# Kernel tuning notes

Measured on AMD Instinct MI355X. Metric: run time of the kernel, lower is better.

## Reference

```python
import jax, jax.numpy as jnp
import numpy as np

B, N, C = 32, 2248, 1024
D = 128            # bottleneck (down_size)
P = 200            # num_prompt_tokens
SCALE = D ** (-0.5)


def setup_inputs() -> dict:
    key = jax.random.key(0)
    k = jax.random.split(key, 5)
    return {
        "x": jax.random.normal(k[0], (B, N, C), dtype=jnp.float32),
        "W_down": jax.random.normal(k[1], (C, D), dtype=jnp.float32) * (C ** -0.5),
        "b_down": jax.random.normal(k[2], (D,), dtype=jnp.float32) * 0.01,
        "W_up": jax.random.normal(k[3], (D, C), dtype=jnp.float32) * (D ** -0.5),
        "b_up": jax.random.normal(k[4], (C,), dtype=jnp.float32) * 0.01,
        "gate": jnp.ones((), dtype=jnp.float32),
    }


def reference(x, W_down, b_down, W_up, b_up, gate):
    # down-projection + exact GELU (torch nn.GELU default is erf-based)
    down = jax.nn.gelu(jnp.einsum('bnc,cd->bnd', x, W_down) + b_down,
                       approximate=False)                      # [B, N, D]
    prompt_down = down[:, :P, :]                               # [B, P, D]
    token_down = down[:, P:, :]                                # [B, N-P, D]
    # prompt-token cross attention
    attn = jax.nn.softmax(
        jnp.einsum('bpd,btd->bpt', prompt_down, token_down) * SCALE, axis=-1)
    prompt_out = jnp.einsum('bpt,btd->bpd', attn, token_down)  # [B, P, D]
    combined = jnp.concatenate([prompt_out, token_down], axis=1)  # [B, N, D]
    up = jnp.einsum('bnd,dc->bnc', combined, W_up) + b_up      # [B, N, C]
    return gate * up
```

## Files before the change

### kernel.cpp

```cpp
#include <hip/hip_runtime.h>
#include <hip/hip_bf16.h>
#include <math.h>

#define B_   32
#define N_   2248
#define C_   1024
#define D_   128
#define P_   200
#define T_   2048
#define M_   (B_ * N_)
#define SCALE_ 0.08838834764831845f

typedef __bf16 bf16;
typedef __bf16 bf16x8 __attribute__((ext_vector_type(8)));
typedef __bf16 bf16x4 __attribute__((ext_vector_type(4)));
typedef float  f32x4  __attribute__((ext_vector_type(4)));
typedef unsigned int u32x4 __attribute__((ext_vector_type(4)));

#define VT_COL(dd, t) ((((((t) >> 3) ^ (((dd) >> 3) & 7)) << 3)) | ((t) & 7))

__device__ __forceinline__ void gl_lds16(const void* g, void* l) {
    __builtin_amdgcn_global_load_lds(
        (const __attribute__((address_space(1))) unsigned int*)g,
        (__attribute__((address_space(3))) unsigned int*)l,
        16, 0, 0);
}

__global__ void k_prep(const float* __restrict__ Wd, const float* __restrict__ Wu,
                       bf16* __restrict__ WtD, bf16* __restrict__ WtU) {
    int i = blockIdx.x * 256 + threadIdx.x;
    if (i >= 131072) return;
    int d = i >> 10, k = i & 1023;
    WtD[i] = (bf16)Wd[k * 128 + d];
    int c = i >> 7, e = i & 127;
    WtU[i] = (bf16)Wu[e * 1024 + c];
}

__launch_bounds__(256, 3)
__global__ void k_down(const float* __restrict__ x, const bf16* __restrict__ WtD,
                       const float* __restrict__ bd, bf16* __restrict__ down) {
    __shared__ __align__(16) char ring[3][16384];
    const int tid = threadIdx.x;
    const int lane = tid & 63, w = tid >> 6;
    const int wm = w >> 1, wn = w & 1;
    const int li = lane & 15, lg = lane >> 4;
    const int m0 = blockIdx.x * 64;

    const int cA0 = w * 2, cA1 = w * 2 + 1;
    const int ar0 = cA0 * 8 + (lane >> 3);
    const int ar1 = cA1 * 8 + (lane >> 3);
    const float* asrc0 = x + (size_t)(m0 + ar0) * C_ + ((((lane & 7) ^ (ar0 & 7)) * 16) >> 2);
    const float* asrc1 = x + (size_t)(m0 + ar1) * C_ + ((((lane & 7) ^ (ar1 & 7)) * 16) >> 2);
    const int br0 = cA0 * 16 + (lane >> 2);
    const int br1 = cA1 * 16 + (lane >> 2);
    const bf16* bsrc0 = WtD + (size_t)br0 * C_ + (((lane & 3) ^ (br0 & 3)) * 8);
    const bf16* bsrc1 = WtD + (size_t)br1 * C_ + (((lane & 3) ^ (br1 & 3)) * 8);

#define STAGE_(t_, s_) do {                                              \
        gl_lds16(asrc0 + (t_) * 32, ring[s_] + cA0 * 1024);              \
        gl_lds16(asrc1 + (t_) * 32, ring[s_] + cA1 * 1024);              \
        gl_lds16(bsrc0 + (t_) * 32, ring[s_] + 8192 + cA0 * 1024);       \
        gl_lds16(bsrc1 + (t_) * 32, ring[s_] + 8192 + cA1 * 1024);       \
    } while (0)

    f32x4 acc[2][4];
    const f32x4 zero = {0.f, 0.f, 0.f, 0.f};
#pragma unroll
    for (int i = 0; i < 2; i++)
#pragma unroll
        for (int j = 0; j < 4; j++) acc[i][j] = zero;

    STAGE_(0, 0);
    STAGE_(1, 1);

    for (int t = 0; t < 32; t++) {
        if (t < 31) { asm volatile("s_waitcnt vmcnt(4)" ::: "memory"); }
        else        { asm volatile("s_waitcnt vmcnt(0)" ::: "memory"); }
        __builtin_amdgcn_sched_barrier(0);
        __builtin_amdgcn_s_barrier();
        __builtin_amdgcn_sched_barrier(0);
        if (t + 2 < 32) {
            int s = (t + 2) % 3;
            STAGE_(t + 2, s);
        }
        const char* sa = ring[t % 3];
        const char* sb = sa + 8192;
        bf16x8 af[2];
#pragma unroll
        for (int f = 0; f < 2; f++) {
            int row = wm * 32 + f * 16 + li;
            const char* rb = sa + row * 128;
            int p0 = (2 * lg) ^ (row & 7), p1 = (2 * lg + 1) ^ (row & 7);
            f32x4 a0 = *(const f32x4*)(rb + p0 * 16);
            f32x4 a1 = *(const f32x4*)(rb + p1 * 16);
            bf16x8 o;
            o[0] = (bf16)a0[0]; o[1] = (bf16)a0[1]; o[2] = (bf16)a0[2]; o[3] = (bf16)a0[3];
            o[4] = (bf16)a1[0]; o[5] = (bf16)a1[1]; o[6] = (bf16)a1[2]; o[7] = (bf16)a1[3];
            af[f] = o;
        }
        bf16x8 bfr[4];
#pragma unroll
        for (int f = 0; f < 4; f++) {
            int row = wn * 64 + f * 16 + li;
            bfr[f] = *(const bf16x8*)(sb + row * 64 + ((lg ^ (row & 3)) * 16));
        }
#pragma unroll
        for (int fm = 0; fm < 2; fm++)
#pragma unroll
            for (int fn = 0; fn < 4; fn++)
                acc[fm][fn] = __builtin_amdgcn_mfma_f32_16x16x32_bf16(
                    af[fm], bfr[fn], acc[fm][fn], 0, 0, 0);
    }
#undef STAGE_

#pragma unroll
    for (int fn = 0; fn < 4; fn++) {
        int col = wn * 64 + fn * 16 + li;
        float bias = bd[col];
#pragma unroll
        for (int fm = 0; fm < 2; fm++) {
            int rb = m0 + wm * 32 + fm * 16 + lg * 4;
#pragma unroll
            for (int r = 0; r < 4; r++) {
                float v = acc[fm][fn][r] + bias;
                float g = 0.5f * v * (1.0f + erff(v * 0.70710678118654752f));
                down[(size_t)(rb + r) * D_ + col] = (bf16)g;
            }
        }
    }
}

__launch_bounds__(256, 3)
__global__ void k_fused(const bf16* __restrict__ down, float* __restrict__ Opart,
                        float* __restrict__ Mpart, float* __restrict__ Lpart,
                        const bf16* __restrict__ WtU, const float* __restrict__ bu,
                        const float* __restrict__ gate, float* __restrict__ out) {
    __shared__ bf16 Ks[64][136];
    __shared__ bf16 Vt[128][72];
    __shared__ bf16 Ps[4][16][72];
    const int tid = threadIdx.x;
    const int lane = tid & 63, w = tid >> 6;
    const int li = lane & 15, lg = lane >> 4;

    if (blockIdx.x < 512) {
        const int bid = blockIdx.x;
        const int wg = (bid & 7) * 64 + (bid >> 3);
        const int b  = wg >> 4;
        const int qt = (wg >> 2) & 3;
        const int th = wg & 3;
        const size_t base = (size_t)b * N_ * D_;
        const int tbase = P_ + th * 512;

        bf16x8 qf[4];
#pragma unroll
        for (int kk = 0; kk < 4; kk++)
            qf[kk] = *(const bf16x8*)(down + base +
                        (size_t)(qt * 64 + w * 16 + li) * D_ + kk * 32 + lg * 8);

        float m_run[4], l_run[4];
        f32x4 acc[8];
        const f32x4 zero = {0.f, 0.f, 0.f, 0.f};
#pragma unroll
        for (int r = 0; r < 4; r++) { m_run[r] = -3.0e38f; l_run[r] = 0.f; }
#pragma unroll
        for (int fn = 0; fn < 8; fn++) acc[fn] = zero;

        for (int tt = 0; tt < 8; tt++) {
            __syncthreads();
#pragma unroll
            for (int it = 0; it < 4; it++) {
                int ch = tid + it * 256;
                int r = ch >> 4, c8 = (ch & 15) * 8;
                u32x4 v = *(const u32x4*)(down + base +
                              (size_t)(tbase + tt * 64 + r) * D_ + c8);
                *(u32x4*)&Ks[r][c8] = v;
                bf16 tmp[8];
                *(u32x4*)tmp = v;
#pragma unroll
                for (int j = 0; j < 8; j++) Vt[c8 + j][VT_COL(c8 + j, r)] = tmp[j];
            }
            __syncthreads();
            f32x4 s[4];
#pragma unroll
            for (int fn = 0; fn < 4; fn++) {
                s[fn] = zero;
#pragma unroll
                for (int kk = 0; kk < 4; kk++) {
                    bf16x8 kf = *(const bf16x8*)&Ks[fn * 16 + li][kk * 32 + lg * 8];
                    s[fn] = __builtin_amdgcn_mfma_f32_16x16x32_bf16(qf[kk], kf, s[fn], 0, 0, 0);
                }
                s[fn] *= SCALE_;
            }
#pragma unroll
            for (int r = 0; r < 4; r++) {
                float tmax = fmaxf(fmaxf(s[0][r], s[1][r]), fmaxf(s[2][r], s[3][r]));
#pragma unroll
                for (int off = 1; off < 16; off <<= 1)
                    tmax = fmaxf(tmax, __shfl_xor(tmax, off, 64));
                float mnew = fmaxf(m_run[r], tmax);
                float corr = __expf(m_run[r] - mnew);
                m_run[r] = mnew;
                float psum = 0.f;
#pragma unroll
                for (int fn = 0; fn < 4; fn++) {
                    float p = __expf(s[fn][r] - mnew);
                    psum += p;
                    Ps[w][lg * 4 + r][fn * 16 + li] = (bf16)p;
                }
#pragma unroll
                for (int off = 1; off < 16; off <<= 1)
                    psum += __shfl_xor(psum, off, 64);
                l_run[r] = l_run[r] * corr + psum;
#pragma unroll
                for (int fn = 0; fn < 8; fn++) acc[fn][r] *= corr;
            }
#pragma unroll
            for (int kk = 0; kk < 2; kk++) {
                bf16x8 pf = *(const bf16x8*)&Ps[w][li][kk * 32 + lg * 8];
#pragma unroll
                for (int fn = 0; fn < 8; fn++) {
                    int d = fn * 16 + li;
                    bf16x8 vf = *(const bf16x8*)&Vt[d][VT_COL(d, kk * 32 + lg * 8)];
                    acc[fn] = __builtin_amdgcn_mfma_f32_16x16x32_bf16(pf, vf, acc[fn], 0, 0, 0);
                }
            }
        }
#pragma unroll
        for (int r = 0; r < 4; r++) {
            int q = qt * 64 + w * 16 + lg * 4 + r;
            size_t ro = ((size_t)(b * 4 + th) * 256 + q) * 128;
#pragma unroll
            for (int fn = 0; fn < 8; fn++)
                Opart[ro + fn * 16 + li] = acc[fn][r];
            if (li == 0) {
                Mpart[(b * 4 + th) * 256 + q] = m_run[r];
                Lpart[(b * 4 + th) * 256 + q] = l_run[r];
            }
        }
    } else {
        const int wm = w >> 1, wn = w & 1;
        int bidu = blockIdx.x - 512;
        int wg = (bidu & 7) * 512 + (bidu >> 3);
        const int b  = wg >> 7;
        const int rt = (wg >> 3) & 15;
        const int nt = wg & 7;
        const size_t m0 = (size_t)b * N_ + P_ + rt * 128;
        const int n0 = nt * 128;

        const bf16* Bp = WtU + (size_t)(n0 + wn * 64 + li) * D_ + lg * 8;

        f32x4 acc[4][4];
        const f32x4 zero = {0.f, 0.f, 0.f, 0.f};
#pragma unroll
        for (int i = 0; i < 4; i++)
#pragma unroll
            for (int j = 0; j < 4; j++) acc[i][j] = zero;

#pragma unroll
        for (int kk = 0; kk < 4; kk++) {
            bf16x8 af[4], bf_[4];
#pragma unroll
            for (int f = 0; f < 4; f++) {
                af[f]  = *(const bf16x8*)(down + (m0 + wm * 64 + f * 16 + li) * D_ + kk * 32 + lg * 8);
                bf_[f] = *(const bf16x8*)(Bp + (size_t)(f * 16) * D_ + kk * 32);
            }
#pragma unroll
            for (int fm = 0; fm < 4; fm++)
#pragma unroll
                for (int fn = 0; fn < 4; fn++)
                    acc[fm][fn] = __builtin_amdgcn_mfma_f32_16x16x32_bf16(
                        af[fm], bf_[fn], acc[fm][fn], 0, 0, 0);
        }

        float g = gate[0];
#pragma unroll
        for (int fn = 0; fn < 4; fn++) {
            int c = n0 + wn * 64 + fn * 16 + li;
            float bias = bu[c];
#pragma unroll
            for (int fm = 0; fm < 4; fm++) {
                size_t rb = m0 + wm * 64 + fm * 16 + lg * 4;
#pragma unroll
                for (int r = 0; r < 4; r++)
                    out[(rb + r) * C_ + c] = g * (acc[fm][fn][r] + bias);
            }
        }
    }
}

__global__ void k_comb(const float* __restrict__ Opart, const float* __restrict__ Mpart,
                       const float* __restrict__ Lpart, bf16* __restrict__ pout) {
    int gid = blockIdx.x * 256 + threadIdx.x;
    if (gid >= (B_ * P_ * D_) / 4) return;
    int e = gid * 4;
    int row = e >> 7;
    int col = e & 127;
    int b = row / P_;
    int q = row - b * P_;
    float mm[4], ll[4];
    float m = -3.0e38f;
#pragma unroll
    for (int t = 0; t < 4; t++) {
        mm[t] = Mpart[(b * 4 + t) * 256 + q];
        ll[t] = Lpart[(b * 4 + t) * 256 + q];
        m = fmaxf(m, mm[t]);
    }
    float a[4], lsum = 0.f;
#pragma unroll
    for (int t = 0; t < 4; t++) { a[t] = __expf(mm[t] - m); lsum += ll[t] * a[t]; }
    float inv = 1.0f / lsum;
    f32x4 o = {0.f, 0.f, 0.f, 0.f};
#pragma unroll
    for (int t = 0; t < 4; t++) {
        f32x4 ot = *(const f32x4*)&Opart[((size_t)(b * 4 + t) * 256 + q) * 128 + col];
#pragma unroll
        for (int j = 0; j < 4; j++) o[j] += ot[j] * a[t];
    }
    bf16x4 ob;
#pragma unroll
    for (int j = 0; j < 4; j++) ob[j] = (bf16)(o[j] * inv);
    *(bf16x4*)&pout[(size_t)row * 128 + col] = ob;
}

__launch_bounds__(256, 3)
__global__ void k_up_prompt(const bf16* __restrict__ pout, const bf16* __restrict__ WtU,
                            const float* __restrict__ bu, const float* __restrict__ gate,
                            float* __restrict__ out) {
    const int tid = threadIdx.x;
    const int lane = tid & 63, wid = tid >> 6;
    const int wm = wid >> 1, wn = wid & 1;
    const int li = lane & 15, lg = lane >> 4;
    const int b  = blockIdx.x >> 4;
    const int pt = (blockIdx.x >> 3) & 1;
    const int nt = blockIdx.x & 7;
    const int n0 = nt * 128;

    const bf16* rp[4];
#pragma unroll
    for (int f = 0; f < 4; f++) {
        int n = pt * 128 + wm * 64 + f * 16 + li;
        int nc = n < P_ ? n : P_ - 1;
        rp[f] = pout + (size_t)(b * P_ + nc) * D_ + lg * 8;
    }
    const bf16* Bp = WtU + (size_t)(n0 + wn * 64 + li) * D_ + lg * 8;

    f32x4 acc[4][4];
    const f32x4 zero = {0.f, 0.f, 0.f, 0.f};
#pragma unroll
    for (int i = 0; i < 4; i++)
#pragma unroll
        for (int j = 0; j < 4; j++) acc[i][j] = zero;

#pragma unroll
    for (int kk = 0; kk < 4; kk++) {
        bf16x8 af[4], bf_[4];
#pragma unroll
        for (int f = 0; f < 4; f++) {
            af[f]  = *(const bf16x8*)(rp[f] + kk * 32);
            bf_[f] = *(const bf16x8*)(Bp + (size_t)(f * 16) * D_ + kk * 32);
        }
#pragma unroll
        for (int fm = 0; fm < 4; fm++)
#pragma unroll
            for (int fn = 0; fn < 4; fn++)
                acc[fm][fn] = __builtin_amdgcn_mfma_f32_16x16x32_bf16(
                    af[fm], bf_[fn], acc[fm][fn], 0, 0, 0);
    }

    float g = gate[0];
#pragma unroll
    for (int fn = 0; fn < 4; fn++) {
        int c = n0 + wn * 64 + fn * 16 + li;
        float bias = bu[c];
#pragma unroll
        for (int fm = 0; fm < 4; fm++) {
            int nr = pt * 128 + wm * 64 + fm * 16 + lg * 4;
#pragma unroll
            for (int r = 0; r < 4; r++) {
                if (nr + r < P_)
                    out[((size_t)b * N_ + nr + r) * C_ + c] = g * (acc[fm][fn][r] + bias);
            }
        }
    }
}

extern "C" void kernel_launch(void* const* d_in, const int* in_sizes, int n_in,
                              void* d_out, int out_size, void* d_ws, size_t ws_size,
                              hipStream_t stream) {
    const float* x    = (const float*)d_in[0];
    const float* Wd   = (const float*)d_in[1];
    const float* bd   = (const float*)d_in[2];
    const float* Wu   = (const float*)d_in[3];
    const float* bu   = (const float*)d_in[4];
    const float* gate = (const float*)d_in[5];
    float* out = (float*)d_out;

    char* w = (char*)d_ws;
    bf16*  down  = (bf16*)w;
    bf16*  pout  = (bf16*)(w + 18415616);
    bf16*  WtD   = (bf16*)(w + 20054016);
    bf16*  WtU   = (bf16*)(w + 20316160);
    float* Opart = (float*)(w + 20578304);
    float* Mpart = (float*)(w + 37355520);
    float* Lpart = (float*)(w + 37486592);

    k_prep<<<512, 256, 0, stream>>>(Wd, Wu, WtD, WtU);
    k_down<<<M_ / 64, 256, 0, stream>>>(x, WtD, bd, down);
    k_fused<<<512 + 4096, 256, 0, stream>>>(down, Opart, Mpart, Lpart,
                                            WtU, bu, gate, out);
    k_comb<<<800, 256, 0, stream>>>(Opart, Mpart, Lpart, pout);
    k_up_prompt<<<512, 256, 0, stream>>>(pout, WtU, bu, gate, out);
}
```

Before: 221.9 us.

## Enlarge down-projection tile to 128 rows and fuse combine into prompt up-projection

The down-projection GEMM tile grows from 64 to 128 rows per block: each wave now computes 64x64 with a larger LDS ring and six async loads per stage, and occupancy drops to 2 blocks per CU. This halves how often W_down is reloaded and raises MFMA work per barrier. Separately, the split-softmax combine kernel is removed and its work (merging the max, sum and partial outputs) is folded into the A-operand load of the prompt up-projection. That drops one launch and the pout round trip, at the cost of redundant combine work across the 8 column tiles.

```diff
diff --git a/kernel.cpp b/kernel.cpp
--- a/kernel.cpp
+++ b/kernel.cpp
@@ -36,37 +36,46 @@
     WtU[i] = (bf16)Wu[e * 1024 + c];
 }
 
-__launch_bounds__(256, 3)
+__launch_bounds__(256, 2)
 __global__ void k_down(const float* __restrict__ x, const bf16* __restrict__ WtD,
                        const float* __restrict__ bd, bf16* __restrict__ down) {
-    __shared__ __align__(16) char ring[3][16384];
+    __shared__ __align__(16) char ring[3][24576];
     const int tid = threadIdx.x;
     const int lane = tid & 63, w = tid >> 6;
     const int wm = w >> 1, wn = w & 1;
     const int li = lane & 15, lg = lane >> 4;
-    const int m0 = blockIdx.x * 64;
-
-    const int cA0 = w * 2, cA1 = w * 2 + 1;
-    const int ar0 = cA0 * 8 + (lane >> 3);
-    const int ar1 = cA1 * 8 + (lane >> 3);
-    const float* asrc0 = x + (size_t)(m0 + ar0) * C_ + ((((lane & 7) ^ (ar0 & 7)) * 16) >> 2);
-    const float* asrc1 = x + (size_t)(m0 + ar1) * C_ + ((((lane & 7) ^ (ar1 & 7)) * 16) >> 2);
-    const int br0 = cA0 * 16 + (lane >> 2);
-    const int br1 = cA1 * 16 + (lane >> 2);
-    const bf16* bsrc0 = WtD + (size_t)br0 * C_ + (((lane & 3) ^ (br0 & 3)) * 8);
-    const bf16* bsrc1 = WtD + (size_t)br1 * C_ + (((lane & 3) ^ (br1 & 3)) * 8);
-
-#define STAGE_(t_, s_) do {                                              \
-        gl_lds16(asrc0 + (t_) * 32, ring[s_] + cA0 * 1024);              \
-        gl_lds16(asrc1 + (t_) * 32, ring[s_] + cA1 * 1024);              \
-        gl_lds16(bsrc0 + (t_) * 32, ring[s_] + 8192 + cA0 * 1024);       \
-        gl_lds16(bsrc1 + (t_) * 32, ring[s_] + 8192 + cA1 * 1024);       \
+    const int m0 = blockIdx.x * 128;
+
+    const float* asrc[4];
+    int ag[4];
+#pragma unroll
+    for (int j = 0; j < 4; j++) {
+        ag[j] = w * 4 + j;
+        int row = ag[j] * 8 + (lane >> 3);
+        asrc[j] = x + (size_t)(m0 + row) * C_ + ((((lane & 7) ^ (row & 7)) * 16) >> 2);
+    }
+    const bf16* bsrc[2];
+    int bg[2];
+#pragma unroll
+    for (int j = 0; j < 2; j++) {
+        bg[j] = w * 2 + j;
+        int row = bg[j] * 16 + (lane >> 2);
+        bsrc[j] = WtD + (size_t)row * C_ + (((lane & 3) ^ (row & 3)) * 8);
+    }
+
+#define STAGE_(t_, s_) do {                                               \
+        gl_lds16(asrc[0] + (t_) * 32, ring[s_] + ag[0] * 1024);           \
+        gl_lds16(asrc[1] + (t_) * 32, ring[s_] + ag[1] * 1024);           \
+        gl_lds16(asrc[2] + (t_) * 32, ring[s_] + ag[2] * 1024);           \
+        gl_lds16(asrc[3] + (t_) * 32, ring[s_] + ag[3] * 1024);           \
+        gl_lds16(bsrc[0] + (t_) * 32, ring[s_] + 16384 + bg[0] * 1024);   \
+        gl_lds16(bsrc[1] + (t_) * 32, ring[s_] + 16384 + bg[1] * 1024);   \
     } while (0)
 
-    f32x4 acc[2][4];
+    f32x4 acc[4][4];
     const f32x4 zero = {0.f, 0.f, 0.f, 0.f};
 #pragma unroll
-    for (int i = 0; i < 2; i++)
+    for (int i = 0; i < 4; i++)
 #pragma unroll
         for (int j = 0; j < 4; j++) acc[i][j] = zero;
 
@@ -74,21 +83,20 @@
     STAGE_(1, 1);
 
     for (int t = 0; t < 32; t++) {
-        if (t < 31) { asm volatile("s_waitcnt vmcnt(4)" ::: "memory"); }
+        if (t < 31) { asm volatile("s_waitcnt vmcnt(6)" ::: "memory"); }
         else        { asm volatile("s_waitcnt vmcnt(0)" ::: "memory"); }
         __builtin_amdgcn_sched_barrier(0);
         __builtin_amdgcn_s_barrier();
         __builtin_amdgcn_sched_barrier(0);
         if (t + 2 < 32) {
-            int s = (t + 2) % 3;
-            STAGE_(t + 2, s);
+            STAGE_(t + 2, (t + 2) % 3);
         }
         const char* sa = ring[t % 3];
-        const char* sb = sa + 8192;
-        bf16x8 af[2];
-#pragma unroll
-        for (int f = 0; f < 2; f++) {
-            int row = wm * 32 + f * 16 + li;
+        const char* sb = sa + 16384;
+        bf16x8 af[4];
+#pragma unroll
+        for (int f = 0; f < 4; f++) {
+            int row = wm * 64 + f * 16 + li;
             const char* rb = sa + row * 128;
             int p0 = (2 * lg) ^ (row & 7), p1 = (2 * lg + 1) ^ (row & 7);
             f32x4 a0 = *(const f32x4*)(rb + p0 * 16);
@@ -105,7 +113,7 @@
             bfr[f] = *(const bf16x8*)(sb + row * 64 + ((lg ^ (row & 3)) * 16));
         }
 #pragma unroll
-        for (int fm = 0; fm < 2; fm++)
+        for (int fm = 0; fm < 4; fm++)
 #pragma unroll
             for (int fn = 0; fn < 4; fn++)
                 acc[fm][fn] = __builtin_amdgcn_mfma_f32_16x16x32_bf16(
@@ -118,8 +126,8 @@
         int col = wn * 64 + fn * 16 + li;
         float bias = bd[col];
 #pragma unroll
-        for (int fm = 0; fm < 2; fm++) {
-            int rb = m0 + wm * 32 + fm * 16 + lg * 4;
+        for (int fm = 0; fm < 4; fm++) {
+            int rb = m0 + wm * 64 + fm * 16 + lg * 4;
 #pragma unroll
             for (int r = 0; r < 4; r++) {
                 float v = acc[fm][fn][r] + bias;
@@ -288,42 +296,9 @@
     }
 }
 
-__global__ void k_comb(const float* __restrict__ Opart, const float* __restrict__ Mpart,
-                       const float* __restrict__ Lpart, bf16* __restrict__ pout) {
-    int gid = blockIdx.x * 256 + threadIdx.x;
-    if (gid >= (B_ * P_ * D_) / 4) return;
-    int e = gid * 4;
-    int row = e >> 7;
-    int col = e & 127;
-    int b = row / P_;
-    int q = row - b * P_;
-    float mm[4], ll[4];
-    float m = -3.0e38f;
-#pragma unroll
-    for (int t = 0; t < 4; t++) {
-        mm[t] = Mpart[(b * 4 + t) * 256 + q];
-        ll[t] = Lpart[(b * 4 + t) * 256 + q];
-        m = fmaxf(m, mm[t]);
-    }
-    float a[4], lsum = 0.f;
-#pragma unroll
-    for (int t = 0; t < 4; t++) { a[t] = __expf(mm[t] - m); lsum += ll[t] * a[t]; }
-    float inv = 1.0f / lsum;
-    f32x4 o = {0.f, 0.f, 0.f, 0.f};
-#pragma unroll
-    for (int t = 0; t < 4; t++) {
-        f32x4 ot = *(const f32x4*)&Opart[((size_t)(b * 4 + t) * 256 + q) * 128 + col];
-#pragma unroll
-        for (int j = 0; j < 4; j++) o[j] += ot[j] * a[t];
-    }
-    bf16x4 ob;
-#pragma unroll
-    for (int j = 0; j < 4; j++) ob[j] = (bf16)(o[j] * inv);
-    *(bf16x4*)&pout[(size_t)row * 128 + col] = ob;
-}
-
-__launch_bounds__(256, 3)
-__global__ void k_up_prompt(const bf16* __restrict__ pout, const bf16* __restrict__ WtU,
+__launch_bounds__(256, 2)
+__global__ void k_up_prompt(const float* __restrict__ Opart, const float* __restrict__ Mpart,
+                            const float* __restrict__ Lpart, const bf16* __restrict__ WtU,
                             const float* __restrict__ bu, const float* __restrict__ gate,
                             float* __restrict__ out) {
     const int tid = threadIdx.x;
@@ -335,12 +310,23 @@
     const int nt = blockIdx.x & 7;
     const int n0 = nt * 128;
 
-    const bf16* rp[4];
+    int qrow[4];
+    float aw[4][4], inv[4];
 #pragma unroll
     for (int f = 0; f < 4; f++) {
         int n = pt * 128 + wm * 64 + f * 16 + li;
-        int nc = n < P_ ? n : P_ - 1;
-        rp[f] = pout + (size_t)(b * P_ + nc) * D_ + lg * 8;
+        qrow[f] = n < P_ ? n : P_ - 1;
+        float mm[4], ll[4], m = -3.0e38f;
+#pragma unroll
+        for (int t = 0; t < 4; t++) {
+            mm[t] = Mpart[(b * 4 + t) * 256 + qrow[f]];
+            ll[t] = Lpart[(b * 4 + t) * 256 + qrow[f]];
+            m = fmaxf(m, mm[t]);
+        }
+        float lsum = 0.f;
+#pragma unroll
+        for (int t = 0; t < 4; t++) { aw[f][t] = __expf(mm[t] - m); lsum += ll[t] * aw[f][t]; }
+        inv[f] = 1.0f / lsum;
     }
     const bf16* Bp = WtU + (size_t)(n0 + wn * 64 + li) * D_ + lg * 8;
 
@@ -356,7 +342,20 @@
         bf16x8 af[4], bf_[4];
 #pragma unroll
         for (int f = 0; f < 4; f++) {
-            af[f]  = *(const bf16x8*)(rp[f] + kk * 32);
+            f32x4 o0 = zero, o1 = zero;
+#pragma unroll
+            for (int t = 0; t < 4; t++) {
+                const float* op = Opart + ((size_t)(b * 4 + t) * 256 + qrow[f]) * 128
+                                  + kk * 32 + lg * 8;
+                f32x4 v0 = *(const f32x4*)op;
+                f32x4 v1 = *(const f32x4*)(op + 4);
+#pragma unroll
+                for (int j = 0; j < 4; j++) { o0[j] += v0[j] * aw[f][t]; o1[j] += v1[j] * aw[f][t]; }
+            }
+            bf16x8 o;
+#pragma unroll
+            for (int j = 0; j < 4; j++) { o[j] = (bf16)(o0[j] * inv[f]); o[j + 4] = (bf16)(o1[j] * inv[f]); }
+            af[f] = o;
             bf_[f] = *(const bf16x8*)(Bp + (size_t)(f * 16) * D_ + kk * 32);
         }
 #pragma unroll
@@ -397,17 +396,15 @@
 
     char* w = (char*)d_ws;
     bf16*  down  = (bf16*)w;
-    bf16*  pout  = (bf16*)(w + 18415616);
-    bf16*  WtD   = (bf16*)(w + 20054016);
-    bf16*  WtU   = (bf16*)(w + 20316160);
-    float* Opart = (float*)(w + 20578304);
-    float* Mpart = (float*)(w + 37355520);
-    float* Lpart = (float*)(w + 37486592);
+    bf16*  WtD   = (bf16*)(w + 18415616);
+    bf16*  WtU   = (bf16*)(w + 18677760);
+    float* Opart = (float*)(w + 18939904);
+    float* Mpart = (float*)(w + 35717120);
+    float* Lpart = (float*)(w + 35848192);
 
     k_prep<<<512, 256, 0, stream>>>(Wd, Wu, WtD, WtU);
-    k_down<<<M_ / 64, 256, 0, stream>>>(x, WtD, bd, down);
+    k_down<<<M_ / 128, 256, 0, stream>>>(x, WtD, bd, down);
     k_fused<<<512 + 4096, 256, 0, stream>>>(down, Opart, Mpart, Lpart,
                                             WtU, bu, gate, out);
-    k_comb<<<800, 256, 0, stream>>>(Opart, Mpart, Lpart, pout);
-    k_up_prompt<<<512, 256, 0, stream>>>(pout, WtU, bu, gate, out);
-}
+    k_up_prompt<<<512, 256, 0, stream>>>(Opart, Mpart, Lpart, WtU, bu, gate, out);
+}
```

New measurement: 268.0 us. +20.8%, slower.
